# Kernel tuning notes

Hardware: AMD Instinct MI355X
Metric: run time of the kernel (lower is better)

## Reference

```python
import jax, jax.numpy as jnp
import numpy as np

HIDDEN = 1024
HEADS = 16
D_HEAD = HIDDEN // HEADS  # 64
N = 2048


def setup_inputs() -> dict:
    key = jax.random.key(0)
    ks = jax.random.split(key, 12)
    s = 1.0 / np.sqrt(HIDDEN)
    return {
        "q": jax.random.normal(ks[0], (N, HIDDEN), jnp.float32),
        "k": jax.random.normal(ks[1], (N, HIDDEN), jnp.float32),
        "v": jax.random.normal(ks[2], (N, HIDDEN), jnp.float32),
        "attn_bias": jax.random.normal(ks[3], (HEADS, 1, N, N), jnp.float32),
        "Wq": jax.random.normal(ks[4], (HIDDEN, HIDDEN), jnp.float32) * s,
        "bq": jax.random.normal(ks[5], (HIDDEN,), jnp.float32) * s,
        "Wk": jax.random.normal(ks[6], (HIDDEN, HIDDEN), jnp.float32) * s,
        "bk": jax.random.normal(ks[7], (HIDDEN,), jnp.float32) * s,
        "Wv": jax.random.normal(ks[8], (HIDDEN, HIDDEN), jnp.float32) * s,
        "bv": jax.random.normal(ks[9], (HIDDEN,), jnp.float32) * s,
        "Wo": jax.random.normal(ks[10], (HIDDEN, HIDDEN), jnp.float32) * s,
        "bo": jax.random.normal(ks[11], (HIDDEN,), jnp.float32) * s,
    }


def reference(q, k, v, attn_bias, Wq, bq, Wk, bk, Wv, bv, Wo, bo):
    # q,k,v: [N, hidden]; attn_bias: [H, 1, N, N]. Attention runs over the
    # node axis (dim 0 in the torch code), inner seq dim is 1 (squeezed).
    n = q.shape[0]
    scale = D_HEAD ** -0.5
    qh = (q @ Wq.T + bq).reshape(n, HEADS, D_HEAD).transpose(1, 0, 2)  # [H,N,d]
    kh = (k @ Wk.T + bk).reshape(n, HEADS, D_HEAD).transpose(1, 0, 2)  # [H,N,d]
    vh = (v @ Wv.T + bv).reshape(n, HEADS, D_HEAD).transpose(1, 0, 2)  # [H,N,d]
    scores = jnp.einsum('hnd,hmd->hnm', qh * scale, kh) + attn_bias[:, 0]  # [H,N,N]
    attn = jax.nn.softmax(scores, axis=-1)
    ctx = jnp.einsum('hnm,hmd->hnd', attn, vh)            # [H,N,d]
    ctx = ctx.transpose(1, 0, 2).reshape(n, HEADS * D_HEAD)  # [N,hidden]
    return ctx @ Wo.T + bo
```

## Files before the change

kernel.cpp:

```cpp
#include <hip/hip_runtime.h>
#include <type_traits>
#include <utility>

#define NT 2048
#define HD 1024
#define NHEAD 16
#define DHEAD 64
#define LOG2E 1.44269504f

typedef float f32x4 __attribute__((ext_vector_type(4)));
typedef __bf16 b16x8 __attribute__((ext_vector_type(8)));
typedef short s16x8 __attribute__((ext_vector_type(8)));
typedef unsigned short u16x8 __attribute__((ext_vector_type(8)));
typedef unsigned short u16x4 __attribute__((ext_vector_type(4)));

template <typename V, typename = void>
struct mfma_takes : std::false_type {};
template <typename V>
struct mfma_takes<V, std::void_t<decltype(__builtin_amdgcn_mfma_f32_16x16x32_bf16(
                         std::declval<V>(), std::declval<V>(), std::declval<f32x4>(), 0, 0, 0))>>
    : std::true_type {};

template <typename V>
__device__ __forceinline__ f32x4 mfma_impl(V a, V b, f32x4 c) {
  return __builtin_amdgcn_mfma_f32_16x16x32_bf16(a, b, c, 0, 0, 0);
}

__device__ __forceinline__ f32x4 mfma_bf16(u16x8 a, u16x8 b, f32x4 c) {
  using V = typename std::conditional<mfma_takes<b16x8>::value, b16x8, s16x8>::type;
  return mfma_impl<V>(__builtin_bit_cast(V, a), __builtin_bit_cast(V, b), c);
}

__device__ __forceinline__ unsigned short f2bf(float f) {
  unsigned int u = __builtin_bit_cast(unsigned int, f);
  return (unsigned short)((u + 0x7FFFu + ((u >> 16) & 1u)) >> 16);
}

__device__ __forceinline__ void gload16(const unsigned short* g, unsigned short* l) {
  __builtin_amdgcn_global_load_lds(
      (__attribute__((address_space(1))) void*)(void*)(g),
      (__attribute__((address_space(3))) void*)(void*)(l), 16, 0, 0);
}

__device__ __forceinline__ void barrier_pinned() {
  __builtin_amdgcn_sched_barrier(0);
  __builtin_amdgcn_s_barrier();
  __builtin_amdgcn_sched_barrier(0);
}
#define WAIT_VM32() asm volatile("s_waitcnt vmcnt(32)" ::: "memory")
#define WAIT_VM8() asm volatile("s_waitcnt vmcnt(8)" ::: "memory")
#define WAIT_VM4() asm volatile("s_waitcnt vmcnt(4)" ::: "memory")
#define WAIT_VM0() asm volatile("s_waitcnt vmcnt(0)" ::: "memory")
#define WAIT_LGKM0() asm volatile("s_waitcnt lgkmcnt(0)" ::: "memory")

__global__ __launch_bounds__(256) void cvt_bf16(
    const float* __restrict__ s0, const float* __restrict__ s1, const float* __restrict__ s2,
    const float* __restrict__ s3,
    unsigned short* __restrict__ d0, unsigned short* __restrict__ d1,
    unsigned short* __restrict__ d2, unsigned short* __restrict__ d3) {
  const int seg = blockIdx.y;
  const float* s;
  unsigned short* d;
  switch (seg) {
    case 0: s = s0; d = d0; break;
    case 1: s = s1; d = d1; break;
    case 2: s = s2; d = d2; break;
    default: s = s3; d = d3; break;
  }
  const int i = blockIdx.x * 2048 + threadIdx.x * 8;
  f32x4 f0 = *reinterpret_cast<const f32x4*>(&s[i]);
  f32x4 f1 = *reinterpret_cast<const f32x4*>(&s[i + 4]);
  u16x8 o;
#pragma unroll
  for (int e = 0; e < 4; ++e) { o[e] = f2bf(f0[e]); o[e + 4] = f2bf(f1[e]); }
  *reinterpret_cast<u16x8*>(&d[i]) = o;
}

__global__ __launch_bounds__(256) void proj_gemm(
    const float* __restrict__ qf32, const float* __restrict__ kf32,
    const float* __restrict__ vf32,
    const unsigned short* __restrict__ Wqb, const unsigned short* __restrict__ Wkb,
    const unsigned short* __restrict__ Wvb,
    const float* __restrict__ bq, const float* __restrict__ bk, const float* __restrict__ bv,
    unsigned short* __restrict__ Qh, unsigned short* __restrict__ Kh,
    unsigned short* __restrict__ Vt) {
  const int L = blockIdx.x;
  const int m = L / 96;
  const int c = L % 96;
  const int z = c / 32;
  const int n = c % 32;
  const int n0 = n * 64, m0 = m * 128;

  const float* A = (z == 0) ? qf32 : (z == 1) ? kf32 : vf32;
  const unsigned short* B = (z == 0) ? Wqb : (z == 1) ? Wkb : Wvb;
  const float* bias = (z == 0) ? bq : (z == 1) ? bk : bv;

  __shared__ unsigned short As0[64 * 64], As1[64 * 64];
  __shared__ unsigned short Bs0[128 * 64], Bs1[128 * 64];

  const int tid = threadIdx.x;
  const int lane = tid & 63;
  const int wr = (tid >> 6) >> 1, wc = (tid >> 6) & 1;
  const int srow = tid >> 3;
  const int schk = (tid & 7) ^ (srow & 7);
  const int scol = schk << 3;

  f32x4 areg[4];

  auto issueA = [&](int kt) {
#pragma unroll
    for (int p = 0; p < 2; ++p) {
      const float* src = &A[(size_t)(n0 + p * 32 + srow) * HD + kt + scol];
      areg[p * 2 + 0] = *reinterpret_cast<const f32x4*>(src);
      areg[p * 2 + 1] = *reinterpret_cast<const f32x4*>(src + 4);
    }
  };
  auto finishA = [&](unsigned short* as) {
#pragma unroll
    for (int p = 0; p < 2; ++p) {
      u16x8 o;
#pragma unroll
      for (int e = 0; e < 4; ++e) {
        o[e] = f2bf(areg[p * 2 + 0][e]);
        o[e + 4] = f2bf(areg[p * 2 + 1][e]);
      }
      *reinterpret_cast<u16x8*>(&as[p * 2048 + tid * 8]) = o;
    }
  };
  auto issueB = [&](int kt, unsigned short* bs) {
#pragma unroll
    for (int p = 0; p < 4; ++p)
      gload16(&B[(size_t)(m0 + p * 32 + srow) * HD + kt + scol], bs + p * 2048 + tid * 8);
  };
  f32x4 acc[2][4] = {};
  auto comp = [&](const unsigned short* as, const unsigned short* bs) {
#pragma unroll
    for (int ks = 0; ks < 2; ++ks) {
      const int q = ks * 4 + (lane >> 4);
      u16x8 a[2], b[4];
#pragma unroll
      for (int i = 0; i < 2; ++i) {
        const int row = wr * 32 + i * 16 + (lane & 15);
        a[i] = *reinterpret_cast<const u16x8*>(&as[row * 64 + ((q ^ (row & 7)) << 3)]);
      }
#pragma unroll
      for (int j = 0; j < 4; ++j) {
        const int row = wc * 64 + j * 16 + (lane & 15);
        b[j] = *reinterpret_cast<const u16x8*>(&bs[row * 64 + ((q ^ (row & 7)) << 3)]);
      }
#pragma unroll
      for (int i = 0; i < 2; ++i)
#pragma unroll
        for (int j = 0; j < 4; ++j)
          acc[i][j] = mfma_bf16(a[i], b[j], acc[i][j]);
    }
  };

  issueA(0);
  issueB(0, Bs0);
  WAIT_VM4();
  finishA(As0);
  issueA(64);
  issueB(64, Bs1);

#pragma unroll 1
  for (int s = 0; s < 14; ++s) {
    WAIT_VM8();
    WAIT_LGKM0();
    barrier_pinned();
    if (s & 1) comp(As1, Bs1); else comp(As0, Bs0);
    barrier_pinned();
    WAIT_VM4();
    finishA((s & 1) ? As0 : As1);
    issueA((s + 2) * 64);
    issueB((s + 2) * 64, (s & 1) ? Bs1 : Bs0);
  }
  WAIT_VM8();
  WAIT_LGKM0();
  barrier_pinned();
  comp(As0, Bs0);
  barrier_pinned();
  WAIT_VM4();
  finishA(As1);
  WAIT_VM0();
  WAIT_LGKM0();
  barrier_pinned();
  comp(As1, Bs1);

  const int rgrp = (lane >> 4) * 4;
  const float scale = (z == 0) ? 0.125f * LOG2E : 1.0f;
#pragma unroll
  for (int i = 0; i < 2; ++i) {
    const int nb = n0 + wr * 32 + i * 16 + rgrp;
#pragma unroll
    for (int j = 0; j < 4; ++j) {
      const int mcol = m0 + wc * 64 + j * 16 + (lane & 15);
      const float bb = bias[mcol];
      if (z == 2) {
        u16x4 pk;
#pragma unroll
        for (int r = 0; r < 4; ++r) pk[r] = f2bf(acc[i][j][r] + bb);
        *reinterpret_cast<u16x4*>(&Vt[(size_t)mcol * NT + nb]) = pk;
      } else {
        unsigned short* dst = (z == 0) ? Qh : Kh;
#pragma unroll
        for (int r = 0; r < 4; ++r)
          dst[(size_t)(nb + r) * HD + mcol] = f2bf((acc[i][j][r] + bb) * scale);
      }
    }
  }
}

__global__ __launch_bounds__(256, 2) void attn_kernel(
    const unsigned short* __restrict__ Qh, const unsigned short* __restrict__ Kh,
    const unsigned short* __restrict__ Vt, const float* __restrict__ bias,
    unsigned short* __restrict__ ctx) {
  const int id = blockIdx.x;
  const int xcd = id & 7, slot = id >> 3;
  const int h = xcd * 2 + (slot >> 5);
  const int q0 = (slot & 31) * 64;
  const int tid = threadIdx.x;
  const int lane = tid & 63;
  const int wave = tid >> 6;

  __shared__ unsigned short Ks0[128 * 64], Ks1[128 * 64];
  __shared__ unsigned short Vs0[64 * 128], Vs1[64 * 128];
  __shared__ unsigned short Ps[4 * 16 * 128];

  u16x8 qf[2];
  {
    const int qrow = q0 + wave * 16 + (lane & 15);
    const int db = (lane >> 4) * 8;
    qf[0] = *reinterpret_cast<const u16x8*>(&Qh[(size_t)qrow * HD + h * DHEAD + db]);
    qf[1] = *reinterpret_cast<const u16x8*>(&Qh[(size_t)qrow * HD + h * DHEAD + 32 + db]);
  }

  f32x4 oacc[4] = {};
  float mrun[4], lrun[4];
#pragma unroll
  for (int r = 0; r < 4; ++r) { mrun[r] = -3.0e38f; lrun[r] = 0.f; }

  const float* bias_h = bias + (size_t)h * NT * NT;
  const int qlrow = q0 + wave * 16 + (lane >> 4) * 4;
  const float* bias_l = bias_h + (size_t)qlrow * NT + (lane & 15);

  const unsigned short* Kbase = Kh + h * DHEAD;
  const unsigned short* Vbase = Vt + (size_t)h * DHEAD * NT;

  const int krow = tid >> 3;
  const int kchk = tid & 7;
  const int vrow = tid >> 4;
  const int vchk = tid & 15;

  auto stage = [&](int t, unsigned short* ks, unsigned short* vs) {
    const int kt = t * 128;
#pragma unroll
    for (int p = 0; p < 4; ++p) {
      const int r = p * 32 + krow;
      gload16(&Kbase[(size_t)(kt + r) * HD + ((kchk ^ (r & 7)) << 3)], ks + p * 2048 + tid * 8);
    }
#pragma unroll
    for (int p = 0; p < 4; ++p) {
      const int r = p * 16 + vrow;
      gload16(&Vbase[(size_t)r * NT + kt + ((vchk ^ (r & 7)) << 3)], vs + p * 2048 + tid * 8);
    }
  };

  float br[8][4];
#pragma unroll
  for (int j = 0; j < 8; ++j)
#pragma unroll
    for (int r = 0; r < 4; ++r) br[j][r] = bias_l[(size_t)r * NT + j * 16];
  stage(0, Ks0, Vs0);
  WAIT_VM0();
  barrier_pinned();

  unsigned short* const psw = Ps + wave * 2048;

#pragma unroll 1
  for (int t = 0; t < NT / 128; ++t) {
    const bool more = (t + 1 < NT / 128);
    const unsigned short* ks = (t & 1) ? Ks1 : Ks0;
    const unsigned short* vs = (t & 1) ? Vs1 : Vs0;

    if (more) stage(t + 1, (t & 1) ? Ks0 : Ks1, (t & 1) ? Vs0 : Vs1);

    f32x4 s[8] = {};
#pragma unroll
    for (int kss = 0; kss < 2; ++kss) {
      const int q = kss * 4 + (lane >> 4);
#pragma unroll
      for (int j = 0; j < 8; ++j) {
        const int row = j * 16 + (lane & 15);
        u16x8 kf = *reinterpret_cast<const u16x8*>(&ks[row * 64 + ((q ^ (row & 7)) << 3)]);
        s[j] = mfma_bf16(qf[kss], kf, s[j]);
      }
    }
#pragma unroll
    for (int j = 0; j < 8; ++j)
#pragma unroll
      for (int r = 0; r < 4; ++r) s[j][r] = fmaf(br[j][r], LOG2E, s[j][r]);

    if (more) {
      const float* bp = bias_l + (size_t)(t + 1) * 128;
#pragma unroll
      for (int j = 0; j < 8; ++j)
#pragma unroll
        for (int r = 0; r < 4; ++r) br[j][r] = bp[(size_t)r * NT + j * 16];
    }

    float mnew[4];
#pragma unroll
    for (int r = 0; r < 4; ++r) {
      float mx = s[0][r];
#pragma unroll
      for (int j = 1; j < 8; ++j) mx = fmaxf(mx, s[j][r]);
      mx = fmaxf(mx, __shfl_xor(mx, 1));
      mx = fmaxf(mx, __shfl_xor(mx, 2));
      mx = fmaxf(mx, __shfl_xor(mx, 4));
      mx = fmaxf(mx, __shfl_xor(mx, 8));
      mnew[r] = fmaxf(mrun[r], mx);
    }
#pragma unroll
    for (int r = 0; r < 4; ++r) {
      const float corr = exp2f(mrun[r] - mnew[r]);
      lrun[r] *= corr;
#pragma unroll
      for (int nd = 0; nd < 4; ++nd) oacc[nd][r] *= corr;
      mrun[r] = mnew[r];
    }
    float psum[4] = {0.f, 0.f, 0.f, 0.f};
#pragma unroll
    for (int j = 0; j < 8; ++j) {
      const int chkbase = j * 2 + ((lane >> 3) & 1);
      const int cofs = lane & 7;
#pragma unroll
      for (int r = 0; r < 4; ++r) {
        const int row = (lane >> 4) * 4 + r;
        const float p = exp2f(s[j][r] - mrun[r]);
        psum[r] += p;
        psw[row * 128 + ((chkbase ^ (row & 7)) << 3) + cofs] = f2bf(p);
      }
    }
#pragma unroll
    for (int r = 0; r < 4; ++r) {
      float tsum = psum[r];
      tsum += __shfl_xor(tsum, 1);
      tsum += __shfl_xor(tsum, 2);
      tsum += __shfl_xor(tsum, 4);
      tsum += __shfl_xor(tsum, 8);
      lrun[r] += tsum;
    }

#pragma unroll
    for (int kk = 0; kk < 4; ++kk) {
      const int q = kk * 4 + (lane >> 4);
      const int prow = lane & 15;
      u16x8 pa = *reinterpret_cast<const u16x8*>(&psw[prow * 128 + ((q ^ (prow & 7)) << 3)]);
#pragma unroll
      for (int nd = 0; nd < 4; ++nd) {
        const int vr = nd * 16 + (lane & 15);
        u16x8 vb = *reinterpret_cast<const u16x8*>(&vs[vr * 128 + ((q ^ (vr & 7)) << 3)]);
        oacc[nd] = mfma_bf16(pa, vb, oacc[nd]);
      }
    }

    WAIT_VM32();
    barrier_pinned();
  }

#pragma unroll
  for (int nd = 0; nd < 4; ++nd) {
#pragma unroll
    for (int r = 0; r < 4; ++r) {
      const float val = oacc[nd][r] / lrun[r];
      ctx[(size_t)(qlrow + r) * HD + h * DHEAD + nd * 16 + (lane & 15)] = f2bf(val);
    }
  }
}

__global__ __launch_bounds__(256) void out_gemm(
    const unsigned short* __restrict__ Ain, const unsigned short* __restrict__ Wob,
    const float* __restrict__ bias, float* __restrict__ out) {
  const int L = blockIdx.x;
  const int m = L / 32;
  const int n = L % 32;
  const int n0 = n * 64, m0 = m * 64;

  __shared__ unsigned short As0[64 * 64], As1[64 * 64];
  __shared__ unsigned short Bs0[64 * 64], Bs1[64 * 64];

  const int tid = threadIdx.x;
  const int lane = tid & 63;
  const int wr = (tid >> 6) >> 1, wc = (tid >> 6) & 1;
  const int srow = tid >> 3;
  const int scol = (((tid & 7) ^ (srow & 7)) << 3);

  auto stage = [&](int kt, unsigned short* as, unsigned short* bs) {
#pragma unroll
    for (int p = 0; p < 2; ++p)
      gload16(&Ain[(size_t)(n0 + p * 32 + srow) * HD + kt + scol], as + p * 2048 + tid * 8);
#pragma unroll
    for (int p = 0; p < 2; ++p)
      gload16(&Wob[(size_t)(m0 + p * 32 + srow) * HD + kt + scol], bs + p * 2048 + tid * 8);
  };
  f32x4 acc[2][2] = {};
  auto comp = [&](const unsigned short* as, const unsigned short* bs) {
#pragma unroll
    for (int ks = 0; ks < 2; ++ks) {
      const int q = ks * 4 + (lane >> 4);
      u16x8 a[2], b[2];
#pragma unroll
      for (int i = 0; i < 2; ++i) {
        const int row = wr * 32 + i * 16 + (lane & 15);
        a[i] = *reinterpret_cast<const u16x8*>(&as[row * 64 + ((q ^ (row & 7)) << 3)]);
      }
#pragma unroll
      for (int j = 0; j < 2; ++j) {
        const int row = wc * 32 + j * 16 + (lane & 15);
        b[j] = *reinterpret_cast<const u16x8*>(&bs[row * 64 + ((q ^ (row & 7)) << 3)]);
      }
#pragma unroll
      for (int i = 0; i < 2; ++i)
#pragma unroll
        for (int j = 0; j < 2; ++j)
          acc[i][j] = mfma_bf16(a[i], b[j], acc[i][j]);
    }
  };

  stage(0, As0, Bs0);
  stage(64, As1, Bs1);
#pragma unroll 1
  for (int s = 0; s < 14; ++s) {
    WAIT_VM4();
    barrier_pinned();
    if (s & 1) comp(As1, Bs1); else comp(As0, Bs0);
    barrier_pinned();
    if (s & 1) stage((s + 2) * 64, As1, Bs1);
    else       stage((s + 2) * 64, As0, Bs0);
  }
  WAIT_VM4();
  barrier_pinned();
  comp(As0, Bs0);
  WAIT_VM0();
  barrier_pinned();
  comp(As1, Bs1);

  const int rgrp = (lane >> 4) * 4;
#pragma unroll
  for (int i = 0; i < 2; ++i) {
    const int nb = n0 + wr * 32 + i * 16 + rgrp;
#pragma unroll
    for (int j = 0; j < 2; ++j) {
      const int mcol = m0 + wc * 32 + j * 16 + (lane & 15);
      const float bb = bias[mcol];
#pragma unroll
      for (int r = 0; r < 4; ++r)
        out[(size_t)(nb + r) * HD + mcol] = acc[i][j][r] + bb;
    }
  }
}

extern "C" void kernel_launch(void* const* d_in, const int* in_sizes, int n_in,
                              void* d_out, int out_size, void* d_ws, size_t ws_size,
                              hipStream_t stream) {
  const float* q  = (const float*)d_in[0];
  const float* k  = (const float*)d_in[1];
  const float* v  = (const float*)d_in[2];
  const float* ab = (const float*)d_in[3];
  const float* Wq = (const float*)d_in[4];
  const float* bq = (const float*)d_in[5];
  const float* Wk = (const float*)d_in[6];
  const float* bk = (const float*)d_in[7];
  const float* Wv = (const float*)d_in[8];
  const float* bv = (const float*)d_in[9];
  const float* Wo = (const float*)d_in[10];
  const float* bo = (const float*)d_in[11];

  unsigned short* Wqb = (unsigned short*)d_ws;
  unsigned short* Wkb = Wqb + (size_t)HD * HD;
  unsigned short* Wvb = Wkb + (size_t)HD * HD;
  unsigned short* Wob = Wvb + (size_t)HD * HD;
  unsigned short* Qh  = Wob + (size_t)HD * HD;
  unsigned short* Kh  = Qh + (size_t)NT * HD;
  unsigned short* Vt  = Kh + (size_t)NT * HD;
  unsigned short* ctx = Vt + (size_t)NT * HD;

  cvt_bf16<<<dim3(512, 4), 256, 0, stream>>>(Wq, Wk, Wv, Wo, Wqb, Wkb, Wvb, Wob);
  proj_gemm<<<dim3(768), 256, 0, stream>>>(
      q, k, v, Wqb, Wkb, Wvb, bq, bk, bv, Qh, Kh, Vt);
  attn_kernel<<<dim3(512), 256, 0, stream>>>(Qh, Kh, Vt, ab, ctx);
  out_gemm<<<dim3(512), 256, 0, stream>>>(ctx, Wob, bo, (float*)d_out);
}
```

Measured before the change: 119.6 us.

## Load A operand directly into MFMA registers, bypassing LDS in projection GEMM

Each wave now loads its fp32 A rows straight from global memory in the MFMA fragment layout, converts them to bf16 in registers, and feeds them to the MFMAs without staging through shared memory. This removes the LDS write and read for A along with the A shared buffers. The loop is unrolled by two with even/odd register buffers, and the vmcnt waits are retuned. Launch bounds now request 3 blocks per CU. The cost is duplicated global A loads across the two column waves, less coalesced access, and more register pressure.

```diff
diff --git a/kernel.cpp b/kernel.cpp
--- a/kernel.cpp
+++ b/kernel.cpp
@@ -48,7 +48,8 @@
   __builtin_amdgcn_sched_barrier(0);
 }
 #define WAIT_VM32() asm volatile("s_waitcnt vmcnt(32)" ::: "memory")
-#define WAIT_VM8() asm volatile("s_waitcnt vmcnt(8)" ::: "memory")
+#define WAIT_VM12() asm volatile("s_waitcnt vmcnt(12)" ::: "memory")
+#define WAIT_VM6() asm volatile("s_waitcnt vmcnt(6)" ::: "memory")
 #define WAIT_VM4() asm volatile("s_waitcnt vmcnt(4)" ::: "memory")
 #define WAIT_VM0() asm volatile("s_waitcnt vmcnt(0)" ::: "memory")
 #define WAIT_LGKM0() asm volatile("s_waitcnt lgkmcnt(0)" ::: "memory")
@@ -76,7 +77,7 @@
   *reinterpret_cast<u16x8*>(&d[i]) = o;
 }
 
-__global__ __launch_bounds__(256) void proj_gemm(
+__global__ __launch_bounds__(256, 3) void proj_gemm(
     const float* __restrict__ qf32, const float* __restrict__ kf32,
     const float* __restrict__ vf32,
     const unsigned short* __restrict__ Wqb, const unsigned short* __restrict__ Wkb,
@@ -95,54 +96,54 @@
   const unsigned short* B = (z == 0) ? Wqb : (z == 1) ? Wkb : Wvb;
   const float* bias = (z == 0) ? bq : (z == 1) ? bk : bv;
 
-  __shared__ unsigned short As0[64 * 64], As1[64 * 64];
   __shared__ unsigned short Bs0[128 * 64], Bs1[128 * 64];
 
   const int tid = threadIdx.x;
   const int lane = tid & 63;
   const int wr = (tid >> 6) >> 1, wc = (tid >> 6) & 1;
   const int srow = tid >> 3;
-  const int schk = (tid & 7) ^ (srow & 7);
-  const int scol = schk << 3;
-
-  f32x4 areg[4];
+  const int scol = (((tid & 7) ^ (srow & 7)) << 3);
+
+  const float* Abase = A + (size_t)(n0 + wr * 32 + (lane & 15)) * HD + ((lane >> 4) << 3);
+
+  f32x4 areg[8];
+  u16x8 abE[4], abO[4];
 
   auto issueA = [&](int kt) {
-#pragma unroll
-    for (int p = 0; p < 2; ++p) {
-      const float* src = &A[(size_t)(n0 + p * 32 + srow) * HD + kt + scol];
-      areg[p * 2 + 0] = *reinterpret_cast<const f32x4*>(src);
-      areg[p * 2 + 1] = *reinterpret_cast<const f32x4*>(src + 4);
-    }
-  };
-  auto finishA = [&](unsigned short* as) {
-#pragma unroll
-    for (int p = 0; p < 2; ++p) {
+    const float* p0 = Abase + kt;
+    const float* p1 = Abase + 16 * HD + kt;
+    areg[0] = *reinterpret_cast<const f32x4*>(p0);
+    areg[1] = *reinterpret_cast<const f32x4*>(p0 + 4);
+    areg[2] = *reinterpret_cast<const f32x4*>(p0 + 32);
+    areg[3] = *reinterpret_cast<const f32x4*>(p0 + 36);
+    areg[4] = *reinterpret_cast<const f32x4*>(p1);
+    areg[5] = *reinterpret_cast<const f32x4*>(p1 + 4);
+    areg[6] = *reinterpret_cast<const f32x4*>(p1 + 32);
+    areg[7] = *reinterpret_cast<const f32x4*>(p1 + 36);
+  };
+  auto cvtA = [&](u16x8 (&ab)[4]) {
+#pragma unroll
+    for (int f = 0; f < 4; ++f) {
       u16x8 o;
 #pragma unroll
       for (int e = 0; e < 4; ++e) {
-        o[e] = f2bf(areg[p * 2 + 0][e]);
-        o[e + 4] = f2bf(areg[p * 2 + 1][e]);
-      }
-      *reinterpret_cast<u16x8*>(&as[p * 2048 + tid * 8]) = o;
-    }
-  };
-  auto issueB = [&](int kt, unsigned short* bs) {
+        o[e] = f2bf(areg[f * 2][e]);
+        o[e + 4] = f2bf(areg[f * 2 + 1][e]);
+      }
+      ab[f] = o;
+    }
+  };
+  auto stageB = [&](int kt, unsigned short* bs) {
 #pragma unroll
     for (int p = 0; p < 4; ++p)
       gload16(&B[(size_t)(m0 + p * 32 + srow) * HD + kt + scol], bs + p * 2048 + tid * 8);
   };
   f32x4 acc[2][4] = {};
-  auto comp = [&](const unsigned short* as, const unsigned short* bs) {
+  auto comp = [&](const u16x8 (&ab)[4], const unsigned short* bs) {
 #pragma unroll
     for (int ks = 0; ks < 2; ++ks) {
       const int q = ks * 4 + (lane >> 4);
-      u16x8 a[2], b[4];
-#pragma unroll
-      for (int i = 0; i < 2; ++i) {
-        const int row = wr * 32 + i * 16 + (lane & 15);
-        a[i] = *reinterpret_cast<const u16x8*>(&as[row * 64 + ((q ^ (row & 7)) << 3)]);
-      }
+      u16x8 b[4];
 #pragma unroll
       for (int j = 0; j < 4; ++j) {
         const int row = wc * 64 + j * 16 + (lane & 15);
@@ -152,40 +153,46 @@
       for (int i = 0; i < 2; ++i)
 #pragma unroll
         for (int j = 0; j < 4; ++j)
-          acc[i][j] = mfma_bf16(a[i], b[j], acc[i][j]);
+          acc[i][j] = mfma_bf16(ab[i * 2 + ks], b[j], acc[i][j]);
     }
   };
 
   issueA(0);
-  issueB(0, Bs0);
+  stageB(0, Bs0);
   WAIT_VM4();
-  finishA(As0);
+  cvtA(abE);
   issueA(64);
-  issueB(64, Bs1);
+  stageB(64, Bs1);
+  WAIT_VM12();
+  barrier_pinned();
 
 #pragma unroll 1
-  for (int s = 0; s < 14; ++s) {
-    WAIT_VM8();
-    WAIT_LGKM0();
-    barrier_pinned();
-    if (s & 1) comp(As1, Bs1); else comp(As0, Bs0);
+  for (int ss = 0; ss < 7; ++ss) {
+    const int s0 = 2 * ss;
+    comp(abE, Bs0);
     barrier_pinned();
     WAIT_VM4();
-    finishA((s & 1) ? As0 : As1);
-    issueA((s + 2) * 64);
-    issueB((s + 2) * 64, (s & 1) ? Bs1 : Bs0);
-  }
-  WAIT_VM8();
-  WAIT_LGKM0();
-  barrier_pinned();
-  comp(As0, Bs0);
+    cvtA(abO);
+    issueA((s0 + 2) * 64);
+    stageB((s0 + 2) * 64, Bs0);
+    WAIT_VM12();
+    barrier_pinned();
+    comp(abO, Bs1);
+    barrier_pinned();
+    WAIT_VM4();
+    cvtA(abE);
+    issueA((s0 + 3) * 64);
+    stageB((s0 + 3) * 64, Bs1);
+    WAIT_VM12();
+    barrier_pinned();
+  }
+  comp(abE, Bs0);
   barrier_pinned();
   WAIT_VM4();
-  finishA(As1);
+  cvtA(abO);
   WAIT_VM0();
-  WAIT_LGKM0();
   barrier_pinned();
-  comp(As1, Bs1);
+  comp(abO, Bs1);
 
   const int rgrp = (lane >> 4) * 4;
   const float scale = (z == 0) ? 0.125f * LOG2E : 1.0f;
```

Measured after the change: 161.8 us. +35.2%, slower.
